# Optimization experiments

Hardware: AMD Instinct MI355X
Metric: run time of the kernel (lower is better)

## Reference

```python
import jax, jax.numpy as jnp
import numpy as np

N = 100_000      # total nodes (1000 graphs x 100 nodes)
E = 1_600_000    # total edges (avg degree 16)
B = 1_000        # ego nodes == batch size
IN_G, HID, H1, HFC, HMLP = 16, 64, 3, 128, 128
D_SENS, D_TGT, D_AREA = 64, 32, 32
OUT_S, OUT_C = 6, 8


def _seg_softmax(e, dst, n):
    # softmax over incoming edges of each destination node; e: [E,H,1]
    m = jax.ops.segment_max(e, dst, num_segments=n)
    ex = jnp.exp(e - m[dst])
    s = jax.ops.segment_sum(ex, dst, num_segments=n)
    return ex / s[dst]


def _egat(feat, efeat, src, dst, Wni, Wnj, Wfij, Wnode, attn, bias, H, d_node, d_edge):
    # DGL EGATConv: f_out = leaky_relu(f_ni[src] + f_nj[dst] + f_fij + bias)
    n = feat.shape[0]
    f_ni = feat @ Wni.T                      # [N, H*d_edge]
    f_nj = feat @ Wnj.T                      # [N, H*d_edge]
    f_e = efeat @ Wfij.T                     # [E, H*d_edge]
    f_out = f_ni[src] + f_nj[dst] + f_e + bias
    f_out = jax.nn.leaky_relu(f_out, 0.01).reshape(-1, H, d_edge)
    e = (f_out * attn).sum(-1, keepdims=True)   # [E,H,1]
    a = _seg_softmax(e, dst, n)                  # edge softmax by dst
    ft = (feat @ Wnode.T).reshape(n, H, d_node)
    h = jax.ops.segment_sum(ft[src] * a, dst, num_segments=n)  # [N,H,d_node]
    return h, f_out


def _ln(x, gamma, beta, eps=1e-5):
    mu = x.mean(-1, keepdims=True)
    v = ((x - mu) ** 2).mean(-1, keepdims=True)
    return (x - mu) * jax.lax.rsqrt(v + eps) * gamma + beta


def setup_inputs() -> dict:
    key = jax.random.key(0)
    ks = jax.random.split(key, 30)
    ego_idx = jnp.arange(0, N, N // B, dtype=jnp.int32)   # one ego node per graph
    feat = jax.random.normal(ks[0], (N, IN_G), jnp.float32)
    feat = feat.at[:, 5].set(0.0).at[ego_idx, 5].set(1.0)  # ego flag column
    enorm = jax.random.uniform(ks[1], (E, 1), dtype=jnp.float32)
    src = jax.random.randint(ks[2], (E,), 0, N, jnp.int32)
    dst = jax.random.randint(ks[3], (E,), 0, N, jnp.int32)
    sensor = jax.random.normal(ks[4], (B, D_SENS), jnp.float32)
    target = jax.random.normal(ks[5], (B, 1, D_TGT), jnp.float32)
    area = jax.random.normal(ks[6], (B, 1, D_AREA), jnp.float32)

    def w(k, o, i):
        return jax.random.normal(k, (o, i), jnp.float32) / np.sqrt(i).astype(np.float32)

    p = {
        'Wni1': w(ks[7], H1, IN_G), 'Wnj1': w(ks[8], H1, IN_G),
        'Wfij1': w(ks[9], H1, 1), 'Wnode1': w(ks[10], H1 * HID, IN_G),
        'attn1': jax.random.normal(ks[11], (1, H1, 1), jnp.float32),
        'bias1': jnp.zeros((H1,), jnp.float32),
        'Wni3': w(ks[12], 1, H1 * HID), 'Wnj3': w(ks[13], 1, H1 * HID),
        'Wfij3': w(ks[14], 1, H1), 'Wnode3': w(ks[15], HFC, H1 * HID),
        'attn3': jax.random.normal(ks[16], (1, 1, 1), jnp.float32),
        'bias3': jnp.zeros((1,), jnp.float32),
        'Ws1': w(ks[17], HMLP, D_SENS), 'bs1': jnp.zeros((HMLP,), jnp.float32),
        'Ws3': w(ks[18], HFC, HMLP), 'bs3': jnp.zeros((HFC,), jnp.float32),
        'Wt1': w(ks[19], HMLP, D_TGT + D_AREA), 'bt1': jnp.zeros((HMLP,), jnp.float32),
        'Wt2': w(ks[20], HFC, HMLP), 'bt2': jnp.zeros((HFC,), jnp.float32),
        'gM': jnp.ones((HMLP,), jnp.float32), 'bM': jnp.zeros((HMLP,), jnp.float32),
        'gF': jnp.ones((HFC,), jnp.float32), 'bF': jnp.zeros((HFC,), jnp.float32),
        'Wfc': w(ks[21], HFC, 3 * HFC), 'bfc': jnp.zeros((HFC,), jnp.float32),
        'Wst': w(ks[22], OUT_S, HFC), 'bst': jnp.zeros((OUT_S,), jnp.float32),
        'Wca': w(ks[23], OUT_C, HFC), 'bca': jnp.zeros((OUT_C,), jnp.float32),
    }
    return {'feat': feat, 'enorm': enorm, 'sensor': sensor, 'target': target,
            'area': area, 'src': src, 'dst': dst, 'ego_idx': ego_idx, **p}


def reference(feat, enorm, sensor, target, area, src, dst, ego_idx,
              Wni1, Wnj1, Wfij1, Wnode1, attn1, bias1,
              Wni3, Wnj3, Wfij3, Wnode3, attn3, bias3,
              Ws1, bs1, Ws3, bs3, Wt1, bt1, Wt2, bt2,
              gM, bM, gF, bF, Wfc, bfc, Wst, bst, Wca, bca):
    relu = jax.nn.relu
    # --- EGAT stack (dropout p=0 -> identity) ---
    hG, hE = _egat(feat, enorm, src, dst, Wni1, Wnj1, Wfij1, Wnode1, attn1, bias1,
                   H1, HID, 1)
    hG = relu(hG.reshape(-1, H1 * HID))          # [N, 192]
    hE = hE.reshape(-1, H1 * 1)                   # [E, 3]
    hG, hE = _egat(hG, hE, src, dst, Wni3, Wnj3, Wfij3, Wnode3, attn3, bias3,
                   1, HFC, 1)
    hG = relu(hG.reshape(-1, HFC))                # [N, 128]
    hGraph = hG[ego_idx]                          # [B, 128] (feat[:,5]==1 nodes)
    # --- sensor MLP ---
    hS = relu(_ln(sensor @ Ws1.T + bs1, gM, bM))
    hS = relu(_ln(hS @ Ws3.T + bs3, gM, bM))
    # --- target MLP ---
    hTA = jnp.concatenate([target[:, 0, :], area[:, 0, :]], axis=1)  # [B, 64]
    hT = relu(_ln(hTA @ Wt1.T + bt1, gM, bM))
    hT = relu(_ln(hT @ Wt2.T + bt2, gM, bM))
    # --- fusion + heads ---
    h = jnp.concatenate([hGraph, hS, hT], axis=1)  # [B, 384]
    h = relu(_ln(h @ Wfc.T + bfc, gF, bF))
    return (h @ Wst.T + bst, h @ Wca.T + bca)
```

## Files before the change

kernel.cpp:

```cpp
#include <hip/hip_runtime.h>
#include <cstdint>

#define N_NODES 100000
#define N_EDGES 1600000
#define N_BATCH 1000
#define LEAK 0.01f
#define MLPB 63
#define RSTRIDE 64

__device__ __forceinline__ float lrelu(float x){ return x > 0.f ? x : LEAK * x; }
__device__ __forceinline__ float expw(float x){ return __expf(fminf(x, 80.f)); }


__global__ void k_pre(const int* __restrict__ ego, int* __restrict__ egoflag, int* __restrict__ Sflag,
                      const float* __restrict__ feat,
                      const float* __restrict__ Wni1, const float* __restrict__ Wnj1,
                      float4* __restrict__ fni1p, float4* __restrict__ fnj1p){
  int n = blockIdx.x * blockDim.x + threadIdx.x;
  if (n < N_BATCH){ int e = ego[n]; egoflag[e] = 1; Sflag[e] = 1; }
  if (n >= N_NODES) return;
  const float4* f4 = (const float4*)(feat + (size_t)n * 16);
  float4 a = f4[0], b = f4[1], c = f4[2], d = f4[3];
  float f[16] = {a.x,a.y,a.z,a.w, b.x,b.y,b.z,b.w, c.x,c.y,c.z,c.w, d.x,d.y,d.z,d.w};
  float ni[3], nj[3];
  #pragma unroll
  for (int h = 0; h < 3; h++){
    float s0 = 0.f, s1 = 0.f;
    #pragma unroll
    for (int k = 0; k < 16; k++){ s0 += f[k] * Wni1[h * 16 + k]; s1 += f[k] * Wnj1[h * 16 + k]; }
    ni[h] = s0; nj[h] = s1;
  }
  fni1p[n] = make_float4(ni[0], ni[1], ni[2], 0.f);
  fnj1p[n] = make_float4(nj[0], nj[1], nj[2], 0.f);
}

__global__ void k_mark_S(const int* __restrict__ src, const int* __restrict__ dst,
                         const int* __restrict__ egoflag, int* __restrict__ Sflag){
  int e4 = blockIdx.x * blockDim.x + threadIdx.x;
  if (e4 >= N_EDGES / 4) return;
  int4 d = ((const int4*)dst)[e4];
  int f0 = egoflag[d.x], f1 = egoflag[d.y], f2 = egoflag[d.z], f3 = egoflag[d.w];
  if (f0 | f1 | f2 | f3){
    int4 s = ((const int4*)src)[e4];
    if (f0) Sflag[s.x] = 1;
    if (f1) Sflag[s.y] = 1;
    if (f2) Sflag[s.z] = 1;
    if (f3) Sflag[s.w] = 1;
  }
}

__global__ void k_compact(const int* __restrict__ Sflag, int* __restrict__ nodeslot,
                          int* __restrict__ S_ids, int* __restrict__ meta){
  int n = blockIdx.x * blockDim.x + threadIdx.x;
  if (n < N_NODES && Sflag[n]){
    int s = atomicAdd(&meta[0], 1);
    S_ids[s] = n; nodeslot[n] = s + 1;
  }
}

__global__ void k_fill(const int* __restrict__ src, const int* __restrict__ dst,
                       const float* __restrict__ enorm,
                       const int* __restrict__ nodeslot, int* __restrict__ cursor,
                       int2* __restrict__ edata){
  int e4 = blockIdx.x * blockDim.x + threadIdx.x;
  if (e4 >= N_EDGES / 4) return;
  int4 d = ((const int4*)dst)[e4];
  int4 s = ((const int4*)src)[e4];
  float4 en = ((const float4*)enorm)[e4];
  int dd[4] = {d.x, d.y, d.z, d.w};
  int ss[4] = {s.x, s.y, s.z, s.w};
  float ee[4] = {en.x, en.y, en.z, en.w};
  #pragma unroll
  for (int u = 0; u < 4; u++){
    int ns = nodeslot[dd[u]];
    if (ns > 0){
      int sl = ns - 1;
      int p = atomicAdd(&cursor[sl], 1);
      if (p < RSTRIDE) edata[sl * RSTRIDE + p] = make_int2(ss[u], __float_as_int(ee[u]));
    }
  }
}


struct L1Sh { float Wn1[192 * 17]; };
struct MlpSh { float Wl[64 * 129]; float act[16 * 64]; float hbuf[16 * 128]; float red[32]; };

__device__ __forceinline__ void sums8(const float* z, float* red, int t, float* s){
  int lane = t & 63, wv = t >> 6, g = t >> 7;
  #pragma unroll
  for (int r = 0; r < 8; r++){
    float a = z[r];
    #pragma unroll
    for (int off = 32; off > 0; off >>= 1) a += __shfl_xor(a, off);
    if (lane == 0) red[wv * 8 + r] = a;
  }
  __syncthreads();
  #pragma unroll
  for (int r = 0; r < 8; r++) s[r] = red[(g * 2) * 8 + r] + red[(g * 2 + 1) * 8 + r];
  __syncthreads();
}

__device__ __forceinline__ void ln_relu8(float* z, float gv, float bv, float* red, int t){
  float s[8];
  sums8(z, red, t, s);
  float d[8], dq[8], q[8];
  #pragma unroll
  for (int r = 0; r < 8; r++){ d[r] = z[r] - s[r] * (1.f / 128.f); dq[r] = d[r] * d[r]; }
  sums8(dq, red, t, q);
  #pragma unroll
  for (int r = 0; r < 8; r++)
    z[r] = fmaxf(0.f, d[r] * rsqrtf(q[r] * (1.f / 128.f) + 1e-5f) * gv + bv);
}

__global__ __launch_bounds__(256) void k6f(
    const float* __restrict__ feat, const float4* __restrict__ fni1p, const float4* __restrict__ fnj1p,
    const int* __restrict__ S_ids, const int* __restrict__ cursor,
    const int2* __restrict__ edata,
    const float* __restrict__ Wnode1, const float* __restrict__ Wfij1,
    const float* __restrict__ attn1, const float* __restrict__ bias1,
    const float* __restrict__ Wni3, const float* __restrict__ Wnj3,
    const int* __restrict__ meta, float* __restrict__ hG_S,
    float* __restrict__ fni3_S, float* __restrict__ fnj3_S,
    const float* __restrict__ sensor, const float* __restrict__ target, const float* __restrict__ area,
    const float* __restrict__ Ws1, const float* __restrict__ bs1,
    const float* __restrict__ Ws3, const float* __restrict__ bs3,
    const float* __restrict__ Wt1, const float* __restrict__ bt1,
    const float* __restrict__ Wt2, const float* __restrict__ bt2,
    const float* __restrict__ gM, const float* __restrict__ bM,
    float* __restrict__ xc_ws)
{
  __shared__ union { L1Sh l1; MlpSh mlp; } sh;
  const int t = threadIdx.x;

  if (blockIdx.x < MLPB){
    const int b0 = blockIdx.x * 16;
    const int o = t & 127, g = t >> 7;
    float g_m = gM[o], b_m = bM[o];
    float* Wl = sh.mlp.Wl; float* act = sh.mlp.act; float* hbuf = sh.mlp.hbuf; float* red = sh.mlp.red;

    for (int i = t; i < 16 * 64; i += 256){
      int r = i >> 6, c = i & 63; int b = b0 + r;
      act[i] = (b < N_BATCH) ? sensor[b * 64 + c] : 0.f;
    }
    for (int i = t; i < 128 * 64; i += 256){
      int oo = i >> 6, cc = i & 63;
      Wl[cc * 129 + oo] = Ws1[i];
    }
    __syncthreads();
    float z[8];
    float bv = bs1[o];
    #pragma unroll
    for (int r = 0; r < 8; r++) z[r] = bv;
    #pragma unroll 4
    for (int c = 0; c < 64; c++){
      float w = Wl[c * 129 + o];
      #pragma unroll
      for (int r = 0; r < 8; r++) z[r] += w * act[(g * 8 + r) * 64 + c];
    }
    ln_relu8(z, g_m, b_m, red, t);
    #pragma unroll
    for (int r = 0; r < 8; r++) hbuf[(g * 8 + r) * 128 + o] = z[r];
    __syncthreads();
    float z2[8];
    bv = bs3[o];
    #pragma unroll
    for (int r = 0; r < 8; r++) z2[r] = bv;
    for (int ch = 0; ch < 2; ch++){
      for (int i = t; i < 128 * 64; i += 256){
        int oo = i >> 6, cc = i & 63;
        Wl[cc * 129 + oo] = Ws3[oo * 128 + ch * 64 + cc];
      }
      __syncthreads();
      #pragma unroll 4
      for (int c = 0; c < 64; c++){
        float w = Wl[c * 129 + o];
        #pragma unroll
        for (int r = 0; r < 8; r++) z2[r] += w * hbuf[(g * 8 + r) * 128 + ch * 64 + c];
      }
      __syncthreads();
    }
    ln_relu8(z2, g_m, b_m, red, t);
    #pragma unroll
    for (int r = 0; r < 8; r++){
      int b = b0 + g * 8 + r;
      if (b < N_BATCH) xc_ws[b * 256 + o] = z2[r];
    }

    for (int i = t; i < 16 * 64; i += 256){
      int r = i >> 6, c = i & 63; int b = b0 + r;
      float v = 0.f;
      if (b < N_BATCH) v = (c < 32) ? target[b * 32 + c] : area[b * 32 + c - 32];
      act[i] = v;
    }
    for (int i = t; i < 128 * 64; i += 256){
      int oo = i >> 6, cc = i & 63;
      Wl[cc * 129 + oo] = Wt1[i];
    }
    __syncthreads();
    bv = bt1[o];
    #pragma unroll
    for (int r = 0; r < 8; r++) z[r] = bv;
    #pragma unroll 4
    for (int c = 0; c < 64; c++){
      float w = Wl[c * 129 + o];
      #pragma unroll
      for (int r = 0; r < 8; r++) z[r] += w * act[(g * 8 + r) * 64 + c];
    }
    ln_relu8(z, g_m, b_m, red, t);
    #pragma unroll
    for (int r = 0; r < 8; r++) hbuf[(g * 8 + r) * 128 + o] = z[r];
    __syncthreads();
    bv = bt2[o];
    #pragma unroll
    for (int r = 0; r < 8; r++) z2[r] = bv;
    for (int ch = 0; ch < 2; ch++){
      for (int i = t; i < 128 * 64; i += 256){
        int oo = i >> 6, cc = i & 63;
        Wl[cc * 129 + oo] = Wt2[oo * 128 + ch * 64 + cc];
      }
      __syncthreads();
      #pragma unroll 4
      for (int c = 0; c < 64; c++){
        float w = Wl[c * 129 + o];
        #pragma unroll
        for (int r = 0; r < 8; r++) z2[r] += w * hbuf[(g * 8 + r) * 128 + ch * 64 + c];
      }
      __syncthreads();
    }
    ln_relu8(z2, g_m, b_m, red, t);
    #pragma unroll
    for (int r = 0; r < 8; r++){
      int b = b0 + g * 8 + r;
      if (b < N_BATCH) xc_ws[b * 256 + 128 + o] = z2[r];
    }
    return;
  }

  float* Wn1 = sh.l1.Wn1;
  for (int i = t; i < 3072; i += 256) Wn1[(i >> 4) * 17 + (i & 15)] = Wnode1[i];
  __syncthreads();
  const int S = meta[0];
  int lane = t & 63;
  int wid = (blockIdx.x - MLPB) * 4 + (t >> 6);
  int nw = (gridDim.x - MLPB) * 4;
  float wf0 = Wfij1[0], wf1 = Wfij1[1], wf2 = Wfij1[2];
  float at0 = attn1[0], at1 = attn1[1], at2 = attn1[2];
  float b0 = bias1[0], b1 = bias1[1], b2 = bias1[2];
  float wi3a = Wni3[lane], wi3b = Wni3[64 + lane], wi3c = Wni3[128 + lane];
  float wj3a = Wnj3[lane], wj3b = Wnj3[64 + lane], wj3c = Wnj3[128 + lane];
  const int e = lane & 15, cg = lane >> 4;

  for (int s = wid; s < S; s += nw){
    int n = S_ids[s];
    int len = min(cursor[s], RSTRIDE);
    long long j0 = (long long)s * RSTRIDE;
    float4 fj = fnj1p[n];
    float ls0 = 0.f, ls1 = 0.f, ls2 = 0.f;
    float ws[3][4];
    #pragma unroll
    for (int h = 0; h < 3; h++)
      #pragma unroll
      for (int k = 0; k < 4; k++) ws[h][k] = 0.f;

    for (int base = 0; base < len; base += 16){
      int idx = base + e;
      if (idx < len){
        int2 ed = edata[j0 + idx];
        int sn = ed.x; float en = __int_as_float(ed.y);
        float4 fi = fni1p[sn];
        float l0 = lrelu(fi.x + fj.x + en * wf0 + b0);
        float l1 = lrelu(fi.y + fj.y + en * wf1 + b1);
        float l2 = lrelu(fi.z + fj.z + en * wf2 + b2);
        float w0 = expw(l0 * at0), w1 = expw(l1 * at1), w2 = expw(l2 * at2);
        ls0 += w0; ls1 += w1; ls2 += w2;
        const float4 f4 = *(const float4*)(feat + (size_t)sn * 16 + cg * 4);
        float fv[4] = {f4.x, f4.y, f4.z, f4.w};
        #pragma unroll
        for (int k = 0; k < 4; k++){
          ws[0][k] += w0 * fv[k];
          ws[1][k] += w1 * fv[k];
          ws[2][k] += w2 * fv[k];
        }
      }
    }
    #pragma unroll
    for (int off = 1; off < 16; off <<= 1){
      ls0 += __shfl_xor(ls0, off);
      ls1 += __shfl_xor(ls1, off);
      ls2 += __shfl_xor(ls2, off);
      #pragma unroll
      for (int h = 0; h < 3; h++)
        #pragma unroll
        for (int k = 0; k < 4; k++) ws[h][k] += __shfl_xor(ws[h][k], off);
    }
    float inv0 = (len > 0) ? 1.f / ls0 : 0.f;
    float inv1 = (len > 0) ? 1.f / ls1 : 0.f;
    float inv2 = (len > 0) ? 1.f / ls2 : 0.f;
    float aval[3][4];
    #pragma unroll
    for (int k = 0; k < 4; k++){
      aval[0][k] = ws[0][k] * inv0;
      aval[1][k] = ws[1][k] * inv1;
      aval[2][k] = ws[2][k] * inv2;
    }
    float hv[3];
    #pragma unroll
    for (int h = 0; h < 3; h++){
      float acc = 0.f;
      #pragma unroll
      for (int q = 0; q < 4; q++)
        #pragma unroll
        for (int k = 0; k < 4; k++)
          acc += __shfl(aval[h][k], q * 16) * Wn1[(h * 64 + lane) * 17 + q * 4 + k];
      hv[h] = fmaxf(acc, 0.f);
      hG_S[(long long)s * 192 + h * 64 + lane] = hv[h];
    }
    float ni = hv[0] * wi3a + hv[1] * wi3b + hv[2] * wi3c;
    float nj = hv[0] * wj3a + hv[1] * wj3b + hv[2] * wj3c;
    #pragma unroll
    for (int off = 32; off > 0; off >>= 1){
      ni += __shfl_xor(ni, off);
      nj += __shfl_xor(nj, off);
    }
    if (lane == 0){ fni3_S[s] = ni; fnj3_S[s] = nj; }
  }
}


__global__ __launch_bounds__(512) void k8f(
    const int* __restrict__ ego, const int* __restrict__ nodeslot, const int* __restrict__ cursor,
    const int2* __restrict__ edata,
    const float4* __restrict__ fni1p, const float4* __restrict__ fnj1p,
    const float* __restrict__ fni3_S, const float* __restrict__ fnj3_S,
    const float* __restrict__ hG_S, const float* __restrict__ Wnode3,
    const float* __restrict__ Wfij1, const float* __restrict__ attn1, const float* __restrict__ bias1,
    const float* __restrict__ Wfij3, const float* __restrict__ attn3, const float* __restrict__ bias3,
    const float* __restrict__ xc_ws,
    const float* __restrict__ gF, const float* __restrict__ bF,
    const float* __restrict__ Wfc, const float* __restrict__ bfc,
    const float* __restrict__ Wst, const float* __restrict__ bst,
    const float* __restrict__ Wca, const float* __restrict__ bca,
    float* __restrict__ out)
{
  __shared__ float Wl[96 * 130];
  __shared__ float agg[8 * 192];
  __shared__ float xc2[8 * 384];
  __shared__ float red[16];
  const int t = threadIdx.x;
  const int lane = t & 63, wv = t >> 6;
  const int o = t & 127, p = t >> 7;

  for (int i = t; i < 8 * 256; i += 512){
    int e = i >> 8, c = i & 255;
    xc2[e * 384 + 128 + c] = xc_ws[(blockIdx.x * 8 + e) * 256 + c];
  }

  {
    int b = blockIdx.x * 8 + wv;
    int n = ego[b];
    int slot = nodeslot[n] - 1;
    int len = min(cursor[slot], RSTRIDE);
    long long j0 = (long long)slot * RSTRIDE;
    float wf0 = Wfij1[0], wf1 = Wfij1[1], wf2 = Wfij1[2];
    float b0 = bias1[0], b1 = bias1[1], b2 = bias1[2];
    float g0 = Wfij3[0], g1 = Wfij3[1], g2 = Wfij3[2];
    float at3 = attn3[0], bb3 = bias3[0];
    float4 fj = fnj1p[n];
    float fnj3v = fnj3_S[slot];

    float lsum = 0.f;
    float acc[3] = {0.f, 0.f, 0.f};
    for (int base = 0; base < len; base += 64){
      int j = base + lane;
      float w = 0.f; int ss = 0;
      if (j < len){
        int2 ed = edata[j0 + j];
        int sn = ed.x; float en = __int_as_float(ed.y);
        float4 fi = fni1p[sn];
        float l0 = lrelu(fi.x + fj.x + en * wf0 + b0);
        float l1 = lrelu(fi.y + fj.y + en * wf1 + b1);
        float l2 = lrelu(fi.z + fj.z + en * wf2 + b2);
        float fe3 = l0 * g0 + l1 * g1 + l2 * g2;
        ss = nodeslot[sn] - 1;
        float l3 = lrelu(fni3_S[ss] + fnj3v + fe3 + bb3);
        w = expw(l3 * at3);
        lsum += w;
      }
      int c2 = min(64, len - base);
      for (int i0 = 0; i0 < c2; i0 += 4){
        float wvv[4], fr[4][3];
        #pragma unroll
        for (int u = 0; u < 4; u++){
          int idx = i0 + u;
          int s2 = __shfl(ss, idx);
          wvv[u] = __shfl(w, idx);
          bool ok = idx < c2;
          #pragma unroll
          for (int r = 0; r < 3; r++)
            fr[u][r] = ok ? hG_S[(long long)s2 * 192 + r * 64 + lane] : 0.f;
          if (!ok) wvv[u] = 0.f;
        }
        #pragma unroll
        for (int u = 0; u < 4; u++)
          #pragma unroll
          for (int r = 0; r < 3; r++) acc[r] += wvv[u] * fr[u][r];
      }
    }
    #pragma unroll
    for (int off = 32; off > 0; off >>= 1) lsum += __shfl_xor(lsum, off);
    float inv = (len > 0) ? 1.f / lsum : 0.f;
    #pragma unroll
    for (int r = 0; r < 3; r++) agg[wv * 192 + r * 64 + lane] = acc[r] * inv;
  }
  __syncthreads();

  {
    float h0 = 0.f, h1 = 0.f;
    for (int ch = 0; ch < 2; ch++){
      for (int i = t; i < 128 * 96; i += 512){
        int oo = i / 96, cc = i - oo * 96;
        Wl[cc * 130 + oo] = Wnode3[oo * 192 + ch * 96 + cc];
      }
      __syncthreads();
      #pragma unroll 8
      for (int c = 0; c < 96; c++){
        float w = Wl[c * 130 + o];
        h0 += w * agg[p * 192 + ch * 96 + c];
        h1 += w * agg[(p + 4) * 192 + ch * 96 + c];
      }
      __syncthreads();
    }
    xc2[p * 384 + o] = fmaxf(0.f, h0);
    xc2[(p + 4) * 384 + o] = fmaxf(0.f, h1);
  }

  float f0 = bfc[o], f1 = f0;
  for (int ch = 0; ch < 4; ch++){
    for (int i = t; i < 128 * 96; i += 512){
      int oo = i / 96, cc = i - oo * 96;
      Wl[cc * 130 + oo] = Wfc[oo * 384 + ch * 96 + cc];
    }
    __syncthreads();
    #pragma unroll 8
    for (int c = 0; c < 96; c++){
      float w = Wl[c * 130 + o];
      f0 += w * xc2[p * 384 + ch * 96 + c];
      f1 += w * xc2[(p + 4) * 384 + ch * 96 + c];
    }
    __syncthreads();
  }

  {
    float a0 = f0, a1 = f1;
    #pragma unroll
    for (int off = 32; off > 0; off >>= 1){ a0 += __shfl_xor(a0, off); a1 += __shfl_xor(a1, off); }
    if (lane == 0){ red[wv * 2] = a0; red[wv * 2 + 1] = a1; }
    __syncthreads();
    float s0 = red[(p * 2) * 2] + red[(p * 2 + 1) * 2];
    float s1 = red[(p * 2) * 2 + 1] + red[(p * 2 + 1) * 2 + 1];
    __syncthreads();
    float d0 = f0 - s0 * (1.f / 128.f), d1 = f1 - s1 * (1.f / 128.f);
    a0 = d0 * d0; a1 = d1 * d1;
    #pragma unroll
    for (int off = 32; off > 0; off >>= 1){ a0 += __shfl_xor(a0, off); a1 += __shfl_xor(a1, off); }
    if (lane == 0){ red[wv * 2] = a0; red[wv * 2 + 1] = a1; }
    __syncthreads();
    float q0 = red[(p * 2) * 2] + red[(p * 2 + 1) * 2];
    float q1 = red[(p * 2) * 2 + 1] + red[(p * 2 + 1) * 2 + 1];
    __syncthreads();
    float gv = gF[o], bv = bF[o];
    f0 = fmaxf(0.f, d0 * rsqrtf(q0 * (1.f / 128.f) + 1e-5f) * gv + bv);
    f1 = fmaxf(0.f, d1 * rsqrtf(q1 * (1.f / 128.f) + 1e-5f) * gv + bv);
  }

  float* v1 = agg;
  v1[p * 128 + o] = f0;
  v1[(p + 4) * 128 + o] = f1;
  for (int i = t; i < 14 * 128; i += 512){
    int oo = i >> 7, cc = i & 127;
    Wl[cc * 15 + oo] = (oo < 6) ? Wst[oo * 128 + cc] : Wca[(oo - 6) * 128 + cc];
  }
  __syncthreads();
  if (o < 14){
    float bb = (o < 6) ? bst[o] : bca[o - 6];
    float a0 = bb, a1 = bb;
    #pragma unroll 8
    for (int c = 0; c < 128; c++){
      float w = Wl[c * 15 + o];
      a0 += w * v1[p * 128 + c];
      a1 += w * v1[(p + 4) * 128 + c];
    }
    int e0 = blockIdx.x * 8 + p, e1 = e0 + 4;
    if (o < 6){
      out[e0 * 6 + o] = a0;
      out[e1 * 6 + o] = a1;
    } else {
      out[N_BATCH * 6 + e0 * 8 + o - 6] = a0;
      out[N_BATCH * 6 + e1 * 8 + o - 6] = a1;
    }
  }
}


extern "C" void kernel_launch(void* const* d_in, const int* in_sizes, int n_in,
                              void* d_out, int out_size, void* d_ws, size_t ws_size,
                              hipStream_t stream)
{
  const float* feat   = (const float*)d_in[0];
  const float* enorm  = (const float*)d_in[1];
  const float* sensor = (const float*)d_in[2];
  const float* target = (const float*)d_in[3];
  const float* area   = (const float*)d_in[4];
  const int*   src    = (const int*)d_in[5];
  const int*   dst    = (const int*)d_in[6];
  const int*   ego    = (const int*)d_in[7];
  const float* Wni1   = (const float*)d_in[8];
  const float* Wnj1   = (const float*)d_in[9];
  const float* Wfij1  = (const float*)d_in[10];
  const float* Wnode1 = (const float*)d_in[11];
  const float* attn1  = (const float*)d_in[12];
  const float* bias1  = (const float*)d_in[13];
  const float* Wni3   = (const float*)d_in[14];
  const float* Wnj3   = (const float*)d_in[15];
  const float* Wfij3  = (const float*)d_in[16];
  const float* Wnode3 = (const float*)d_in[17];
  const float* attn3  = (const float*)d_in[18];
  const float* bias3  = (const float*)d_in[19];
  const float* Ws1    = (const float*)d_in[20];
  const float* bs1    = (const float*)d_in[21];
  const float* Ws3    = (const float*)d_in[22];
  const float* bs3    = (const float*)d_in[23];
  const float* Wt1    = (const float*)d_in[24];
  const float* bt1    = (const float*)d_in[25];
  const float* Wt2    = (const float*)d_in[26];
  const float* bt2    = (const float*)d_in[27];
  const float* gM     = (const float*)d_in[28];
  const float* bM     = (const float*)d_in[29];
  const float* gF     = (const float*)d_in[30];
  const float* bF     = (const float*)d_in[31];
  const float* Wfc    = (const float*)d_in[32];
  const float* bfc    = (const float*)d_in[33];
  const float* Wst    = (const float*)d_in[34];
  const float* bst    = (const float*)d_in[35];
  const float* Wca    = (const float*)d_in[36];
  const float* bca    = (const float*)d_in[37];
  float* out = (float*)d_out;

  char* ws = (char*)d_ws;
  size_t off = 0;
  auto alloc = [&](size_t bytes) -> size_t {
    size_t o = off;
    off = (off + bytes + 255) & ~(size_t)255;
    return o;
  };

  size_t o_meta    = alloc(256);
  size_t o_egoflag = alloc((size_t)N_NODES * 4);
  size_t o_Sflag   = alloc((size_t)N_NODES * 4);
  size_t o_nodeslot= alloc((size_t)N_NODES * 4);
  size_t o_cursor  = alloc((size_t)N_NODES * 4);
  size_t zero_bytes = off;
  size_t o_fni1p   = alloc((size_t)N_NODES * 16);
  size_t o_fnj1p   = alloc((size_t)N_NODES * 16);
  size_t o_S_ids   = alloc((size_t)N_NODES * 4);
  size_t o_fni3    = alloc((size_t)N_NODES * 4);
  size_t o_fnj3    = alloc((size_t)N_NODES * 4);
  size_t o_xc      = alloc((size_t)N_BATCH * 256 * 4);
  size_t rem = (ws_size > off) ? ws_size - off : 0;
  size_t scap = rem / (RSTRIDE * 8 + 768);
  if (scap > (size_t)N_NODES) scap = N_NODES;
  if (scap < 1) scap = 1;
  size_t o_edata = alloc(scap * RSTRIDE * 8);
  size_t o_hG_S  = alloc(scap * 768);

  int*    meta      = (int*)(ws + o_meta);
  int*    egoflag   = (int*)(ws + o_egoflag);
  int*    Sflag     = (int*)(ws + o_Sflag);
  int*    nodeslot  = (int*)(ws + o_nodeslot);
  int*    cursor    = (int*)(ws + o_cursor);
  float4* fni1p     = (float4*)(ws + o_fni1p);
  float4* fnj1p     = (float4*)(ws + o_fnj1p);
  int*    S_ids     = (int*)(ws + o_S_ids);
  float*  fni3_S    = (float*)(ws + o_fni3);
  float*  fnj3_S    = (float*)(ws + o_fnj3);
  float*  xc_ws     = (float*)(ws + o_xc);
  int2*   edata     = (int2*)(ws + o_edata);
  float*  hG_S      = (float*)(ws + o_hG_S);

  hipMemsetAsync(ws, 0, zero_bytes, stream);

  k_pre<<<(N_NODES + 255) / 256, 256, 0, stream>>>(ego, egoflag, Sflag, feat, Wni1, Wnj1, fni1p, fnj1p);
  k_mark_S<<<(N_EDGES / 4 + 255) / 256, 256, 0, stream>>>(src, dst, egoflag, Sflag);
  k_compact<<<(N_NODES + 255) / 256, 256, 0, stream>>>(Sflag, nodeslot, S_ids, meta);
  k_fill<<<(N_EDGES / 4 + 255) / 256, 256, 0, stream>>>(src, dst, enorm, nodeslot, cursor, edata);
  k6f<<<MLPB + 2048, 256, 0, stream>>>(feat, fni1p, fnj1p, S_ids, cursor, edata,
                                       Wnode1, Wfij1, attn1, bias1, Wni3, Wnj3, meta,
                                       hG_S, fni3_S, fnj3_S,
                                       sensor, target, area, Ws1, bs1, Ws3, bs3,
                                       Wt1, bt1, Wt2, bt2, gM, bM, xc_ws);
  k8f<<<N_BATCH / 8, 512, 0, stream>>>(ego, nodeslot, cursor, edata, fni1p, fnj1p,
                                       fni3_S, fnj3_S, hG_S, Wnode3,
                                       Wfij1, attn1, bias1, Wfij3, attn3, bias3,
                                       xc_ws, gF, bF, Wfc, bfc, Wst, bst, Wca, bca, out);
  (void)in_sizes; (void)n_in; (void)out_size;
}
```

Before: 273.0 us.

## Move sensor/target MLP into k_fill and halve k8f per-block batch

The sensor and target MLP blocks move out of the layer-1 EGAT kernel and into the edge-fill kernel. This lets k6f drop its large shared-memory union, which should raise its occupancy, and lets the MLP run alongside the edge bucketing. The MLP weights are now staged into shared memory in 8-column chunks, trading a much smaller LDS footprint for many more barriers. k8f now handles 4 ego nodes per 256-thread block instead of 8 per 512, which doubles the block count to fill more CUs but loads each weight tile twice as often overall.

```diff
diff --git a/kernel.cpp b/kernel.cpp
--- a/kernel.cpp
+++ b/kernel.cpp
@@ -58,11 +58,132 @@
   }
 }
 
-__global__ void k_fill(const int* __restrict__ src, const int* __restrict__ dst,
-                       const float* __restrict__ enorm,
-                       const int* __restrict__ nodeslot, int* __restrict__ cursor,
-                       int2* __restrict__ edata){
-  int e4 = blockIdx.x * blockDim.x + threadIdx.x;
+
+struct FillSh {
+  float act[16 * 64];
+  float hbuf[16 * 128];
+  float Wc[8 * 129];
+  float red[32];
+};
+
+__device__ __forceinline__ void sums8(const float* z, float* red, int t, float* s){
+  int lane = t & 63, wv = t >> 6, g = t >> 7;
+  #pragma unroll
+  for (int r = 0; r < 8; r++){
+    float a = z[r];
+    #pragma unroll
+    for (int off = 32; off > 0; off >>= 1) a += __shfl_xor(a, off);
+    if (lane == 0) red[wv * 8 + r] = a;
+  }
+  __syncthreads();
+  #pragma unroll
+  for (int r = 0; r < 8; r++) s[r] = red[(g * 2) * 8 + r] + red[(g * 2 + 1) * 8 + r];
+  __syncthreads();
+}
+
+__device__ __forceinline__ void ln_relu8(float* z, float gv, float bv, float* red, int t){
+  float s[8];
+  sums8(z, red, t, s);
+  float d[8], dq[8], q[8];
+  #pragma unroll
+  for (int r = 0; r < 8; r++){ d[r] = z[r] - s[r] * (1.f / 128.f); dq[r] = d[r] * d[r]; }
+  sums8(dq, red, t, q);
+  #pragma unroll
+  for (int r = 0; r < 8; r++)
+    z[r] = fmaxf(0.f, d[r] * rsqrtf(q[r] * (1.f / 128.f) + 1e-5f) * gv + bv);
+}
+
+template<int K>
+__device__ __forceinline__ void mlp_layer(const float* __restrict__ Wg, const float* in_lds,
+                                          float* Wc, float* z, int t, int o, int g){
+  for (int ch = 0; ch < K / 8; ch++){
+    __syncthreads();
+    for (int i = t; i < 128 * 8; i += 256){
+      int oo = i >> 3, cc = i & 7;
+      Wc[cc * 129 + oo] = Wg[oo * K + ch * 8 + cc];
+    }
+    __syncthreads();
+    #pragma unroll
+    for (int c = 0; c < 8; c++){
+      float w = Wc[c * 129 + o];
+      #pragma unroll
+      for (int r = 0; r < 8; r++) z[r] += w * in_lds[(g * 8 + r) * K + ch * 8 + c];
+    }
+  }
+  __syncthreads();
+}
+
+__global__ __launch_bounds__(256) void k_fill(
+    const int* __restrict__ src, const int* __restrict__ dst,
+    const float* __restrict__ enorm,
+    const int* __restrict__ nodeslot, int* __restrict__ cursor,
+    int2* __restrict__ edata,
+    const float* __restrict__ sensor, const float* __restrict__ target, const float* __restrict__ area,
+    const float* __restrict__ Ws1, const float* __restrict__ bs1,
+    const float* __restrict__ Ws3, const float* __restrict__ bs3,
+    const float* __restrict__ Wt1, const float* __restrict__ bt1,
+    const float* __restrict__ Wt2, const float* __restrict__ bt2,
+    const float* __restrict__ gM, const float* __restrict__ bM,
+    float* __restrict__ xc_ws)
+{
+  __shared__ FillSh sh;
+  const int t = threadIdx.x;
+
+  if (blockIdx.x < MLPB){
+    const int b0 = blockIdx.x * 16;
+    const int o = t & 127, g = t >> 7;
+    float g_m = gM[o], b_m = bM[o];
+    float z[8], z2[8];
+
+    for (int i = t; i < 16 * 64; i += 256){
+      int r = i >> 6, c = i & 63; int b = b0 + r;
+      sh.act[i] = (b < N_BATCH) ? sensor[b * 64 + c] : 0.f;
+    }
+    { float bv = bs1[o];
+      #pragma unroll
+      for (int r = 0; r < 8; r++) z[r] = bv; }
+    mlp_layer<64>(Ws1, sh.act, sh.Wc, z, t, o, g);
+    ln_relu8(z, g_m, b_m, sh.red, t);
+    #pragma unroll
+    for (int r = 0; r < 8; r++) sh.hbuf[(g * 8 + r) * 128 + o] = z[r];
+    { float bv = bs3[o];
+      #pragma unroll
+      for (int r = 0; r < 8; r++) z2[r] = bv; }
+    mlp_layer<128>(Ws3, sh.hbuf, sh.Wc, z2, t, o, g);
+    ln_relu8(z2, g_m, b_m, sh.red, t);
+    #pragma unroll
+    for (int r = 0; r < 8; r++){
+      int b = b0 + g * 8 + r;
+      if (b < N_BATCH) xc_ws[b * 256 + o] = z2[r];
+    }
+
+    for (int i = t; i < 16 * 64; i += 256){
+      int r = i >> 6, c = i & 63; int b = b0 + r;
+      float v = 0.f;
+      if (b < N_BATCH) v = (c < 32) ? target[b * 32 + c] : area[b * 32 + c - 32];
+      sh.act[i] = v;
+    }
+    { float bv = bt1[o];
+      #pragma unroll
+      for (int r = 0; r < 8; r++) z[r] = bv; }
+    mlp_layer<64>(Wt1, sh.act, sh.Wc, z, t, o, g);
+    ln_relu8(z, g_m, b_m, sh.red, t);
+    #pragma unroll
+    for (int r = 0; r < 8; r++) sh.hbuf[(g * 8 + r) * 128 + o] = z[r];
+    { float bv = bt2[o];
+      #pragma unroll
+      for (int r = 0; r < 8; r++) z2[r] = bv; }
+    mlp_layer<128>(Wt2, sh.hbuf, sh.Wc, z2, t, o, g);
+    ln_relu8(z2, g_m, b_m, sh.red, t);
+    #pragma unroll
+    for (int r = 0; r < 8; r++){
+      int b = b0 + g * 8 + r;
+      if (b < N_BATCH) xc_ws[b * 256 + 128 + o] = z2[r];
+    }
+    return;
+  }
+
+  int e4 = (blockIdx.x - MLPB) * 256 + t;
   if (e4 >= N_EDGES / 4) return;
   int4 d = ((const int4*)dst)[e4];
   int4 s = ((const int4*)src)[e4];
@@ -82,36 +203,6 @@
 }
 
 
-struct L1Sh { float Wn1[192 * 17]; };
-struct MlpSh { float Wl[64 * 129]; float act[16 * 64]; float hbuf[16 * 128]; float red[32]; };
-
-__device__ __forceinline__ void sums8(const float* z, float* red, int t, float* s){
-  int lane = t & 63, wv = t >> 6, g = t >> 7;
-  #pragma unroll
-  for (int r = 0; r < 8; r++){
-    float a = z[r];
-    #pragma unroll
-    for (int off = 32; off > 0; off >>= 1) a += __shfl_xor(a, off);
-    if (lane == 0) red[wv * 8 + r] = a;
-  }
-  __syncthreads();
-  #pragma unroll
-  for (int r = 0; r < 8; r++) s[r] = red[(g * 2) * 8 + r] + red[(g * 2 + 1) * 8 + r];
-  __syncthreads();
-}
-
-__device__ __forceinline__ void ln_relu8(float* z, float gv, float bv, float* red, int t){
-  float s[8];
-  sums8(z, red, t, s);
-  float d[8], dq[8], q[8];
-  #pragma unroll
-  for (int r = 0; r < 8; r++){ d[r] = z[r] - s[r] * (1.f / 128.f); dq[r] = d[r] * d[r]; }
-  sums8(dq, red, t, q);
-  #pragma unroll
-  for (int r = 0; r < 8; r++)
-    z[r] = fmaxf(0.f, d[r] * rsqrtf(q[r] * (1.f / 128.f) + 1e-5f) * gv + bv);
-}
-
 __global__ __launch_bounds__(256) void k6f(
     const float* __restrict__ feat, const float4* __restrict__ fni1p, const float4* __restrict__ fnj1p,
     const int* __restrict__ S_ids, const int* __restrict__ cursor,
@@ -120,129 +211,16 @@
     const float* __restrict__ attn1, const float* __restrict__ bias1,
     const float* __restrict__ Wni3, const float* __restrict__ Wnj3,
     const int* __restrict__ meta, float* __restrict__ hG_S,
-    float* __restrict__ fni3_S, float* __restrict__ fnj3_S,
-    const float* __restrict__ sensor, const float* __restrict__ target, const float* __restrict__ area,
-    const float* __restrict__ Ws1, const float* __restrict__ bs1,
-    const float* __restrict__ Ws3, const float* __restrict__ bs3,
-    const float* __restrict__ Wt1, const float* __restrict__ bt1,
-    const float* __restrict__ Wt2, const float* __restrict__ bt2,
-    const float* __restrict__ gM, const float* __restrict__ bM,
-    float* __restrict__ xc_ws)
+    float* __restrict__ fni3_S, float* __restrict__ fnj3_S)
 {
-  __shared__ union { L1Sh l1; MlpSh mlp; } sh;
+  __shared__ float Wn1[192 * 17];
   const int t = threadIdx.x;
-
-  if (blockIdx.x < MLPB){
-    const int b0 = blockIdx.x * 16;
-    const int o = t & 127, g = t >> 7;
-    float g_m = gM[o], b_m = bM[o];
-    float* Wl = sh.mlp.Wl; float* act = sh.mlp.act; float* hbuf = sh.mlp.hbuf; float* red = sh.mlp.red;
-
-    for (int i = t; i < 16 * 64; i += 256){
-      int r = i >> 6, c = i & 63; int b = b0 + r;
-      act[i] = (b < N_BATCH) ? sensor[b * 64 + c] : 0.f;
-    }
-    for (int i = t; i < 128 * 64; i += 256){
-      int oo = i >> 6, cc = i & 63;
-      Wl[cc * 129 + oo] = Ws1[i];
-    }
-    __syncthreads();
-    float z[8];
-    float bv = bs1[o];
-    #pragma unroll
-    for (int r = 0; r < 8; r++) z[r] = bv;
-    #pragma unroll 4
-    for (int c = 0; c < 64; c++){
-      float w = Wl[c * 129 + o];
-      #pragma unroll
-      for (int r = 0; r < 8; r++) z[r] += w * act[(g * 8 + r) * 64 + c];
-    }
-    ln_relu8(z, g_m, b_m, red, t);
-    #pragma unroll
-    for (int r = 0; r < 8; r++) hbuf[(g * 8 + r) * 128 + o] = z[r];
-    __syncthreads();
-    float z2[8];
-    bv = bs3[o];
-    #pragma unroll
-    for (int r = 0; r < 8; r++) z2[r] = bv;
-    for (int ch = 0; ch < 2; ch++){
-      for (int i = t; i < 128 * 64; i += 256){
-        int oo = i >> 6, cc = i & 63;
-        Wl[cc * 129 + oo] = Ws3[oo * 128 + ch * 64 + cc];
-      }
-      __syncthreads();
-      #pragma unroll 4
-      for (int c = 0; c < 64; c++){
-        float w = Wl[c * 129 + o];
-        #pragma unroll
-        for (int r = 0; r < 8; r++) z2[r] += w * hbuf[(g * 8 + r) * 128 + ch * 64 + c];
-      }
-      __syncthreads();
-    }
-    ln_relu8(z2, g_m, b_m, red, t);
-    #pragma unroll
-    for (int r = 0; r < 8; r++){
-      int b = b0 + g * 8 + r;
-      if (b < N_BATCH) xc_ws[b * 256 + o] = z2[r];
-    }
-
-    for (int i = t; i < 16 * 64; i += 256){
-      int r = i >> 6, c = i & 63; int b = b0 + r;
-      float v = 0.f;
-      if (b < N_BATCH) v = (c < 32) ? target[b * 32 + c] : area[b * 32 + c - 32];
-      act[i] = v;
-    }
-    for (int i = t; i < 128 * 64; i += 256){
-      int oo = i >> 6, cc = i & 63;
-      Wl[cc * 129 + oo] = Wt1[i];
-    }
-    __syncthreads();
-    bv = bt1[o];
-    #pragma unroll
-    for (int r = 0; r < 8; r++) z[r] = bv;
-    #pragma unroll 4
-    for (int c = 0; c < 64; c++){
-      float w = Wl[c * 129 + o];
-      #pragma unroll
-      for (int r = 0; r < 8; r++) z[r] += w * act[(g * 8 + r) * 64 + c];
-    }
-    ln_relu8(z, g_m, b_m, red, t);
-    #pragma unroll
-    for (int r = 0; r < 8; r++) hbuf[(g * 8 + r) * 128 + o] = z[r];
-    __syncthreads();
-    bv = bt2[o];
-    #pragma unroll
-    for (int r = 0; r < 8; r++) z2[r] = bv;
-    for (int ch = 0; ch < 2; ch++){
-      for (int i = t; i < 128 * 64; i += 256){
-        int oo = i >> 6, cc = i & 63;
-        Wl[cc * 129 + oo] = Wt2[oo * 128 + ch * 64 + cc];
-      }
-      __syncthreads();
-      #pragma unroll 4
-      for (int c = 0; c < 64; c++){
-        float w = Wl[c * 129 + o];
-        #pragma unroll
-        for (int r = 0; r < 8; r++) z2[r] += w * hbuf[(g * 8 + r) * 128 + ch * 64 + c];
-      }
-      __syncthreads();
-    }
-    ln_relu8(z2, g_m, b_m, red, t);
-    #pragma unroll
-    for (int r = 0; r < 8; r++){
-      int b = b0 + g * 8 + r;
-      if (b < N_BATCH) xc_ws[b * 256 + 128 + o] = z2[r];
-    }
-    return;
-  }
-
-  float* Wn1 = sh.l1.Wn1;
   for (int i = t; i < 3072; i += 256) Wn1[(i >> 4) * 17 + (i & 15)] = Wnode1[i];
   __syncthreads();
   const int S = meta[0];
   int lane = t & 63;
-  int wid = (blockIdx.x - MLPB) * 4 + (t >> 6);
-  int nw = (gridDim.x - MLPB) * 4;
+  int wid = blockIdx.x * 4 + (t >> 6);
+  int nw = gridDim.x * 4;
   float wf0 = Wfij1[0], wf1 = Wfij1[1], wf2 = Wfij1[2];
   float at0 = attn1[0], at1 = attn1[1], at2 = attn1[2];
   float b0 = bias1[0], b1 = bias1[1], b2 = bias1[2];
@@ -327,7 +305,7 @@
 }
 
 
-__global__ __launch_bounds__(512) void k8f(
+__global__ __launch_bounds__(256) void k8f(
     const int* __restrict__ ego, const int* __restrict__ nodeslot, const int* __restrict__ cursor,
     const int2* __restrict__ edata,
     const float4* __restrict__ fni1p, const float4* __restrict__ fnj1p,
@@ -342,21 +320,21 @@
     const float* __restrict__ Wca, const float* __restrict__ bca,
     float* __restrict__ out)
 {
-  __shared__ float Wl[96 * 130];
-  __shared__ float agg[8 * 192];
-  __shared__ float xc2[8 * 384];
+  __shared__ float Wl[48 * 130];
+  __shared__ float agg[4 * 192];
+  __shared__ float xc2[4 * 384];
   __shared__ float red[16];
   const int t = threadIdx.x;
   const int lane = t & 63, wv = t >> 6;
   const int o = t & 127, p = t >> 7;
 
-  for (int i = t; i < 8 * 256; i += 512){
+  for (int i = t; i < 4 * 256; i += 256){
     int e = i >> 8, c = i & 255;
-    xc2[e * 384 + 128 + c] = xc_ws[(blockIdx.x * 8 + e) * 256 + c];
+    xc2[e * 384 + 128 + c] = xc_ws[(blockIdx.x * 4 + e) * 256 + c];
   }
 
   {
-    int b = blockIdx.x * 8 + wv;
+    int b = blockIdx.x * 4 + wv;
     int n = ego[b];
     int slot = nodeslot[n] - 1;
     int len = min(cursor[slot], RSTRIDE);
@@ -416,36 +394,36 @@
 
   {
     float h0 = 0.f, h1 = 0.f;
-    for (int ch = 0; ch < 2; ch++){
-      for (int i = t; i < 128 * 96; i += 512){
-        int oo = i / 96, cc = i - oo * 96;
-        Wl[cc * 130 + oo] = Wnode3[oo * 192 + ch * 96 + cc];
+    for (int ch = 0; ch < 4; ch++){
+      for (int i = t; i < 128 * 48; i += 256){
+        int oo = i / 48, cc = i - oo * 48;
+        Wl[cc * 130 + oo] = Wnode3[oo * 192 + ch * 48 + cc];
       }
       __syncthreads();
       #pragma unroll 8
-      for (int c = 0; c < 96; c++){
+      for (int c = 0; c < 48; c++){
         float w = Wl[c * 130 + o];
-        h0 += w * agg[p * 192 + ch * 96 + c];
-        h1 += w * agg[(p + 4) * 192 + ch * 96 + c];
+        h0 += w * agg[p * 192 + ch * 48 + c];
+        h1 += w * agg[(p + 2) * 192 + ch * 48 + c];
       }
       __syncthreads();
     }
     xc2[p * 384 + o] = fmaxf(0.f, h0);
-    xc2[(p + 4) * 384 + o] = fmaxf(0.f, h1);
+    xc2[(p + 2) * 384 + o] = fmaxf(0.f, h1);
   }
 
   float f0 = bfc[o], f1 = f0;
-  for (int ch = 0; ch < 4; ch++){
-    for (int i = t; i < 128 * 96; i += 512){
-      int oo = i / 96, cc = i - oo * 96;
-      Wl[cc * 130 + oo] = Wfc[oo * 384 + ch * 96 + cc];
+  for (int ch = 0; ch < 8; ch++){
+    for (int i = t; i < 128 * 48; i += 256){
+      int oo = i / 48, cc = i - oo * 48;
+      Wl[cc * 130 + oo] = Wfc[oo * 384 + ch * 48 + cc];
     }
     __syncthreads();
     #pragma unroll 8
-    for (int c = 0; c < 96; c++){
+    for (int c = 0; c < 48; c++){
       float w = Wl[c * 130 + o];
-      f0 += w * xc2[p * 384 + ch * 96 + c];
-      f1 += w * xc2[(p + 4) * 384 + ch * 96 + c];
+      f0 += w * xc2[p * 384 + ch * 48 + c];
+      f1 += w * xc2[(p + 2) * 384 + ch * 48 + c];
     }
     __syncthreads();
   }
@@ -475,8 +453,8 @@
 
   float* v1 = agg;
   v1[p * 128 + o] = f0;
-  v1[(p + 4) * 128 + o] = f1;
-  for (int i = t; i < 14 * 128; i += 512){
+  v1[(p + 2) * 128 + o] = f1;
+  for (int i = t; i < 14 * 128; i += 256){
     int oo = i >> 7, cc = i & 127;
     Wl[cc * 15 + oo] = (oo < 6) ? Wst[oo * 128 + cc] : Wca[(oo - 6) * 128 + cc];
   }
@@ -488,9 +466,9 @@
     for (int c = 0; c < 128; c++){
       float w = Wl[c * 15 + o];
       a0 += w * v1[p * 128 + c];
-      a1 += w * v1[(p + 4) * 128 + c];
-    }
-    int e0 = blockIdx.x * 8 + p, e1 = e0 + 4;
+      a1 += w * v1[(p + 2) * 128 + c];
+    }
+    int e0 = blockIdx.x * 4 + p, e1 = e0 + 2;
     if (o < 6){
       out[e0 * 6 + o] = a0;
       out[e1 * 6 + o] = a1;
@@ -592,13 +570,13 @@
   k_pre<<<(N_NODES + 255) / 256, 256, 0, stream>>>(ego, egoflag, Sflag, feat, Wni1, Wnj1, fni1p, fnj1p);
   k_mark_S<<<(N_EDGES / 4 + 255) / 256, 256, 0, stream>>>(src, dst, egoflag, Sflag);
   k_compact<<<(N_NODES + 255) / 256, 256, 0, stream>>>(Sflag, nodeslot, S_ids, meta);
-  k_fill<<<(N_EDGES / 4 + 255) / 256, 256, 0, stream>>>(src, dst, enorm, nodeslot, cursor, edata);
-  k6f<<<MLPB + 2048, 256, 0, stream>>>(feat, fni1p, fnj1p, S_ids, cursor, edata,
-                                       Wnode1, Wfij1, attn1, bias1, Wni3, Wnj3, meta,
-                                       hG_S, fni3_S, fnj3_S,
-                                       sensor, target, area, Ws1, bs1, Ws3, bs3,
-                                       Wt1, bt1, Wt2, bt2, gM, bM, xc_ws);
-  k8f<<<N_BATCH / 8, 512, 0, stream>>>(ego, nodeslot, cursor, edata, fni1p, fnj1p,
+  k_fill<<<MLPB + (N_EDGES / 4 + 255) / 256, 256, 0, stream>>>(
+      src, dst, enorm, nodeslot, cursor, edata,
+      sensor, target, area, Ws1, bs1, Ws3, bs3, Wt1, bt1, Wt2, bt2, gM, bM, xc_ws);
+  k6f<<<2048, 256, 0, stream>>>(feat, fni1p, fnj1p, S_ids, cursor, edata,
+                                Wnode1, Wfij1, attn1, bias1, Wni3, Wnj3, meta,
+                                hG_S, fni3_S, fnj3_S);
+  k8f<<<N_BATCH / 4, 256, 0, stream>>>(ego, nodeslot, cursor, edata, fni1p, fnj1p,
                                        fni3_S, fnj3_S, hG_S, Wnode3,
                                        Wfij1, attn1, bias1, Wfij3, attn3, bias3,
                                        xc_ws, gF, bF, Wfc, bfc, Wst, bst, Wca, bca, out);
```

Measured after the change: 343.9 us. 1.26x slower.
